# Kernel tuning notes

Measured on AMD Instinct MI355X. Metric: run time of the kernel, lower is better.

Reference implementation:

```python
import jax, jax.numpy as jnp
import numpy as np

BN_EPS = 1e-5


def conv1x1(x, W, b):
    # x: [B, Cin, N], W: [Cout, Cin], b: [Cout]
    return jnp.einsum('bcn,oc->bon', x, W) + b[None, :, None]


def batchnorm(x, gamma, beta):
    # training-mode BatchNorm1d over (batch, spatial) for x: [B, C, N]
    m = jnp.mean(x, axis=(0, 2), keepdims=True)
    v = jnp.var(x, axis=(0, 2), keepdims=True)
    return (x - m) * jax.lax.rsqrt(v + BN_EPS) * gamma[None, :, None] + beta[None, :, None]


def square_distance(a, b):
    # a: [B, N, 3], b: [B, S, 3] -> [B, N, S]
    aa = jnp.sum(a * a, axis=-1, keepdims=True)        # [B,N,1]
    bb = jnp.sum(b * b, axis=-1)[:, None, :]           # [B,1,S]
    return aa + bb - 2.0 * jnp.einsum('bnc,bsc->bns', a, b)


def setup_inputs() -> dict:
    key = jax.random.key(0)
    ks = jax.random.split(key, 16)
    B, N, S = 4, 8192, 2048
    D1, D2 = 128, 256
    Cin, Cout = D1 + D2, 256
    hid = Cout  # res_expansion = 1.0
    inp = {
        'xyz1': jax.random.normal(ks[0], (B, N, 3), jnp.float32),
        'xyz2': jax.random.normal(ks[1], (B, S, 3), jnp.float32),
        'points1': jax.random.normal(ks[2], (B, D1, N), jnp.float32),
        'points2': jax.random.normal(ks[3], (B, D2, S), jnp.float32),
        # fuse: Conv1d(Cin->Cout,k=1) + BN + ReLU
        'W_fuse': jax.random.normal(ks[4], (Cout, Cin), jnp.float32) * (1.0 / np.sqrt(Cin)),
        'b_fuse': jnp.zeros((Cout,), jnp.float32),
        'g_fuse': jnp.ones((Cout,), jnp.float32),
        'be_fuse': jnp.zeros((Cout,), jnp.float32),
        # extraction residual block: conv1 -> bn -> relu -> conv2 -> bn, +res, relu
        'W1': jax.random.normal(ks[5], (hid, Cout), jnp.float32) * (1.0 / np.sqrt(Cout)),
        'b1': jnp.zeros((hid,), jnp.float32),
        'g1': jnp.ones((hid,), jnp.float32),
        'be1': jnp.zeros((hid,), jnp.float32),
        'W2': jax.random.normal(ks[6], (Cout, hid), jnp.float32) * (1.0 / np.sqrt(hid)),
        'b2': jnp.zeros((Cout,), jnp.float32),
        'g2': jnp.ones((Cout,), jnp.float32),
        'be2': jnp.zeros((Cout,), jnp.float32),
    }
    return inp


def reference(xyz1, xyz2, points1, points2,
              W_fuse, b_fuse, g_fuse, be_fuse,
              W1, b1, g1, be1, W2, b2, g2, be2):
    B, N, _ = xyz1.shape
    p2 = jnp.transpose(points2, (0, 2, 1))  # [B, S, D2]
    # 3-NN inverse-distance interpolation
    dists = square_distance(xyz1, xyz2)                 # [B, N, S]
    neg_d3, idx = jax.lax.top_k(-dists, 3)              # 3 smallest distances
    d3 = -neg_d3                                        # [B, N, 3]
    recip = 1.0 / (d3 + 1e-8)
    weight = recip / jnp.sum(recip, axis=2, keepdims=True)  # [B, N, 3]
    gathered = jax.vmap(lambda pts, i: pts[i])(p2, idx)     # [B, N, 3, D2]
    interp = jnp.sum(gathered * weight[..., None], axis=2)  # [B, N, D2]
    # concat skip features
    p1 = jnp.transpose(points1, (0, 2, 1))              # [B, N, D1]
    new_points = jnp.concatenate([p1, interp], axis=-1) # [B, N, D1+D2]
    x = jnp.transpose(new_points, (0, 2, 1))            # [B, Cin, N]
    # fuse: ConvBNReLU1D
    x = jax.nn.relu(batchnorm(conv1x1(x, W_fuse, b_fuse), g_fuse, be_fuse))
    # extraction: residual ConvBNReLURes1D block
    y = jax.nn.relu(batchnorm(conv1x1(x, W1, b1), g1, be1))
    y = batchnorm(conv1x1(y, W2, b2), g2, be2)
    return jax.nn.relu(x + y)
```

## Files before the change

kernel.cpp:

```cpp
#include <hip/hip_runtime.h>
#include <cstdint>
#include <cstddef>

#define B_ 4
#define N_ 8192
#define S_ 2048
#define M_ 32768

typedef short bf16x8 __attribute__((ext_vector_type(8)));
typedef float f32x4 __attribute__((ext_vector_type(4)));

__device__ __forceinline__ float bf2f(unsigned short u) {
  union { unsigned int i; float f; } v; v.i = ((unsigned int)u) << 16; return v.f;
}
__device__ __forceinline__ unsigned short f2bf(float f) {
  union { float f; unsigned int i; } v; v.f = f;
  return (unsigned short)((v.i + 0x7FFFu + ((v.i >> 16) & 1u)) >> 16);
}

__global__ void pack_weights(const float* __restrict__ Wf, const float* __restrict__ W1,
                             const float* __restrict__ W2, unsigned short* __restrict__ out) {
  int i = blockIdx.x * 256 + threadIdx.x;
  float v;
  if (i < 98304)       v = Wf[i];
  else if (i < 163840) v = W1[i - 98304];
  else                 v = W2[i - 163840];
  out[i] = f2bf(v);
}

__global__ void transpose_to_bf16(const float* __restrict__ src, unsigned short* __restrict__ dst,
                                  int C, int Nsp, int ldo, int coff) {
  __shared__ float t[32][33];
  int b = blockIdx.z;
  int n0 = blockIdx.x * 32, c0 = blockIdx.y * 32;
  int x = threadIdx.x, y = threadIdx.y;
  const float* s = src + ((size_t)b * C + c0) * Nsp + n0;
#pragma unroll
  for (int k = 0; k < 4; ++k)
    t[y + k * 8][x] = s[(size_t)(y + k * 8) * Nsp + x];
  __syncthreads();
#pragma unroll
  for (int k = 0; k < 4; ++k) {
    int n = n0 + y + k * 8;
    dst[((size_t)b * Nsp + n) * ldo + coff + c0 + x] = f2bf(t[x][y + k * 8]);
  }
}

__device__ __forceinline__ bool lexlt(float da, int ia, float db, int ib) {
  return (da < db) || (da == db && ia < ib);
}

__global__ __launch_bounds__(256, 8) void knn_interp_kernel(
    const float* __restrict__ xyz1, const float* __restrict__ xyz2,
    const unsigned short* __restrict__ p2t, unsigned short* __restrict__ np) {
  __shared__ float4 sp[1024];
  __shared__ float sw[16][3];
  __shared__ int   sidx[16][3];
  int t = threadIdx.x;
  int b = blockIdx.y;
  const float* xb = xyz2 + (size_t)b * S_ * 3;

  int lane = t & 63, wave = t >> 6;
  int sub = lane & 15;
  int pib = wave * 4 + (lane >> 4);
  int n = blockIdx.x * 16 + pib;
  const float* q = xyz1 + ((size_t)b * N_ + n) * 3;
  float px = q[0], py = q[1], pz = q[2];
  float nx = -2.f * px, ny = -2.f * py, nz = -2.f * pz;
  float aa = fmaf(px, px, fmaf(py, py, pz * pz));

  float d0 = 1e30f, d1 = 1e30f, d2 = 1e30f;
  int i0 = S_, i1 = S_, i2 = S_;

  for (int chunk = 0; chunk < 2; ++chunk) {
    __syncthreads();
    for (int i = t; i < 1024; i += 256) {
      int c = chunk * 1024 + i;
      float cx = xb[3 * c], cy = xb[3 * c + 1], cz = xb[3 * c + 2];
      sp[i] = make_float4(cx, cy, cz, fmaf(cx, cx, fmaf(cy, cy, cz * cz)));
    }
    __syncthreads();
    int sbase = chunk * 1024;
#pragma unroll 4
    for (int i = 0; i < 64; ++i) {
      int sl = i * 16 + sub;
      float4 c = sp[sl];
      float d = fmaf(nx, c.x, fmaf(ny, c.y, fmaf(nz, c.z, c.w)));
      int s = sbase + sl;
      bool b0 = d < d0, b1 = d < d1, b2 = d < d2;
      d2 = b1 ? d1 : (b2 ? d : d2);
      i2 = b1 ? i1 : (b2 ? s : i2);
      d1 = b0 ? d0 : (b1 ? d : d1);
      i1 = b0 ? i0 : (b1 ? s : i1);
      d0 = b0 ? d : d0;
      i0 = b0 ? s : i0;
    }
  }

#pragma unroll
  for (int m = 1; m <= 8; m <<= 1) {
    float e0 = __shfl_xor(d0, m, 64), e1 = __shfl_xor(d1, m, 64), e2 = __shfl_xor(d2, m, 64);
    int   j0 = __shfl_xor(i0, m, 64), j1 = __shfl_xor(i1, m, 64), j2 = __shfl_xor(i2, m, 64);
    bool l0 = lexlt(d0, i0, e0, j0);
    float m0d = l0 ? d0 : e0;  int m0i = l0 ? i0 : j0;
    float x0d = l0 ? e0 : d0;  int x0i = l0 ? j0 : i0;
    bool l11 = lexlt(d1, i1, e1, j1);
    float n1d = l11 ? d1 : e1; int n1i = l11 ? i1 : j1;
    bool l1 = lexlt(n1d, n1i, x0d, x0i);
    float m1d = l1 ? n1d : x0d; int m1i = l1 ? n1i : x0i;
    bool l01 = lexlt(d0, i0, e1, j1);
    float p1d = l01 ? e1 : d0; int p1i = l01 ? j1 : i0;
    bool l10 = lexlt(d1, i1, e0, j0);
    float p2d = l10 ? e0 : d1; int p2i = l10 ? j0 : i1;
    bool lp = lexlt(p1d, p1i, p2d, p2i);
    float p3d = lp ? p1d : p2d; int p3i = lp ? p1i : p2i;
    bool l22 = lexlt(d2, i2, e2, j2);
    float p4d = l22 ? d2 : e2; int p4i = l22 ? i2 : j2;
    bool l2 = lexlt(p3d, p3i, p4d, p4i);
    float m2d = l2 ? p3d : p4d; int m2i = l2 ? p3i : p4i;
    d0 = m0d; i0 = m0i; d1 = m1d; i1 = m1i; d2 = m2d; i2 = m2i;
  }

  if (sub == 0) {
    float t0 = aa + d0, t1 = aa + d1, t2 = aa + d2;
    float r0 = 1.f / (t0 + 1e-8f), r1 = 1.f / (t1 + 1e-8f), r2 = 1.f / (t2 + 1e-8f);
    float rs = 1.f / (r0 + r1 + r2);
    sw[pib][0] = r0 * rs; sw[pib][1] = r1 * rs; sw[pib][2] = r2 * rs;
    sidx[pib][0] = i0; sidx[pib][1] = i1; sidx[pib][2] = i2;
  }
  __syncthreads();

  for (int p = wave; p < 16; p += 4) {
    float w0 = sw[p][0], w1 = sw[p][1], w2 = sw[p][2];
    const ushort4* g0 = (const ushort4*)(p2t + ((size_t)b * S_ + sidx[p][0]) * 256) + lane;
    const ushort4* g1 = (const ushort4*)(p2t + ((size_t)b * S_ + sidx[p][1]) * 256) + lane;
    const ushort4* g2 = (const ushort4*)(p2t + ((size_t)b * S_ + sidx[p][2]) * 256) + lane;
    ushort4 a = *g0, c = *g1, e = *g2;
    ushort4 o;
    o.x = f2bf(w0 * bf2f(a.x) + w1 * bf2f(c.x) + w2 * bf2f(e.x));
    o.y = f2bf(w0 * bf2f(a.y) + w1 * bf2f(c.y) + w2 * bf2f(e.y));
    o.z = f2bf(w0 * bf2f(a.z) + w1 * bf2f(c.z) + w2 * bf2f(e.z));
    o.w = f2bf(w0 * bf2f(a.w) + w1 * bf2f(c.w) + w2 * bf2f(e.w));
    int nn = blockIdx.x * 16 + p;
    *((ushort4*)(np + ((size_t)b * N_ + nn) * 384 + 128) + lane) = o;
  }
}

__global__ __launch_bounds__(256) void gemm_bt(const unsigned short* __restrict__ A,
                                               const unsigned short* __restrict__ Bw,
                                               float* __restrict__ C, int K) {
  __shared__ unsigned short As[128 * 64];
  __shared__ unsigned short Bs[128 * 64];
  int tid = threadIdx.x;
  int lane = tid & 63, wave = tid >> 6;
  int wr = wave >> 1, wc = wave & 1;
  size_t m0 = (size_t)blockIdx.x * 128;
  int n0 = blockIdx.y * 128;
  int lr = lane & 15, lk = lane >> 4;
  f32x4 acc[4][4] = {};

  for (int kt = 0; kt < K; kt += 64) {
#pragma unroll
    for (int i = 0; i < 4; ++i) {
      int ch = i * 256 + tid;
      int row = ch >> 3;
      int col = (ch & 7) * 8;
      __builtin_amdgcn_global_load_lds(
          (const __attribute__((address_space(1))) void*)(A + (m0 + row) * K + kt + col),
          (__attribute__((address_space(3))) void*)(As + ch * 8), 16, 0, 0);
    }
#pragma unroll
    for (int i = 0; i < 4; ++i) {
      int ch = i * 256 + tid;
      int row = ch >> 3;
      int col = (ch & 7) * 8;
      __builtin_amdgcn_global_load_lds(
          (const __attribute__((address_space(1))) void*)(Bw + (size_t)(n0 + row) * K + kt + col),
          (__attribute__((address_space(3))) void*)(Bs + ch * 8), 16, 0, 0);
    }
    __syncthreads();

    bf16x8 af[4][2], bf[4][2];
#pragma unroll
    for (int m = 0; m < 4; ++m)
#pragma unroll
      for (int kk = 0; kk < 2; ++kk)
        af[m][kk] = *(const bf16x8*)(As + (wr * 64 + m * 16 + lr) * 64 + kk * 32 + lk * 8);
#pragma unroll
    for (int nn = 0; nn < 4; ++nn)
#pragma unroll
      for (int kk = 0; kk < 2; ++kk)
        bf[nn][kk] = *(const bf16x8*)(Bs + (wc * 64 + nn * 16 + lr) * 64 + kk * 32 + lk * 8);

#pragma unroll
    for (int m = 0; m < 4; ++m)
#pragma unroll
      for (int nn = 0; nn < 4; ++nn)
#pragma unroll
        for (int kk = 0; kk < 2; ++kk)
          acc[m][nn] = __builtin_amdgcn_mfma_f32_16x16x32_bf16(af[m][kk], bf[nn][kk], acc[m][nn], 0, 0, 0);
    __syncthreads();
  }

#pragma unroll
  for (int m = 0; m < 4; ++m) {
    size_t row = m0 + wr * 64 + m * 16 + lk * 4;
#pragma unroll
    for (int j = 0; j < 4; ++j) {
      float* cr = C + (row + j) * 256 + n0 + wc * 64 + lr;
#pragma unroll
      for (int nn = 0; nn < 4; ++nn)
        cr[nn * 16] = acc[m][nn][j];
    }
  }
}

__global__ void col_stats(const float* __restrict__ X, float* __restrict__ sums) {
  int c = threadIdx.x;
  size_t r0 = (size_t)blockIdx.x * 256;
  float s0 = 0, s1 = 0, s2 = 0, s3 = 0, q0 = 0, q1 = 0, q2 = 0, q3 = 0;
  for (int r = 0; r < 256; r += 4) {
    float v0 = X[(r0 + r + 0) * 256 + c];
    float v1 = X[(r0 + r + 1) * 256 + c];
    float v2 = X[(r0 + r + 2) * 256 + c];
    float v3 = X[(r0 + r + 3) * 256 + c];
    s0 += v0; q0 += v0 * v0;
    s1 += v1; q1 += v1 * v1;
    s2 += v2; q2 += v2 * v2;
    s3 += v3; q3 += v3 * v3;
  }
  atomicAdd(&sums[c], s0 + s1 + s2 + s3);
  atomicAdd(&sums[256 + c], q0 + q1 + q2 + q3);
}

__global__ void bn_relu_kernel(const float* __restrict__ X, const float* __restrict__ sums,
                               const float* __restrict__ g, const float* __restrict__ be,
                               unsigned short* __restrict__ Y) {
  __shared__ float sc[256], sh[256];
  int t = threadIdx.x;
  {
    float s = sums[t], q = sums[256 + t];
    float m = s * (1.0f / 32768.0f);
    float v = q * (1.0f / 32768.0f) - m * m;
    float scale = g[t] * rsqrtf(v + 1e-5f);
    sc[t] = scale; sh[t] = be[t] - m * scale;
  }
  __syncthreads();
  const float4* X4 = (const float4*)X;
  ushort4* Y4 = (ushort4*)Y;
  for (size_t i = (size_t)blockIdx.x * 256 + t; i < (size_t)M_ * 64; i += 2048 * 256) {
    float4 x = X4[i];
    int c0 = (int)((i * 4) & 255);
    ushort4 o;
    o.x = f2bf(fmaxf(x.x * sc[c0 + 0] + sh[c0 + 0], 0.f));
    o.y = f2bf(fmaxf(x.y * sc[c0 + 1] + sh[c0 + 1], 0.f));
    o.z = f2bf(fmaxf(x.z * sc[c0 + 2] + sh[c0 + 2], 0.f));
    o.w = f2bf(fmaxf(x.w * sc[c0 + 3] + sh[c0 + 3], 0.f));
    Y4[i] = o;
  }
}

__global__ void final_kernel(const float* __restrict__ Z, const unsigned short* __restrict__ Xb,
                             const float* __restrict__ sums2, const float* __restrict__ g2,
                             const float* __restrict__ be2, float* __restrict__ out) {
  __shared__ float sc[64], sh[64];
  __shared__ float tile[64 * 65];
  int t = threadIdx.x;
  int o0 = blockIdx.y * 64;
  if (t < 64) {
    int c = o0 + t;
    float s = sums2[c], q = sums2[256 + c];
    float m = s * (1.0f / 32768.0f);
    float v = q * (1.0f / 32768.0f) - m * m;
    float scale = g2[c] * rsqrtf(v + 1e-5f);
    sc[t] = scale; sh[t] = be2[c] - m * scale;
  }
  __syncthreads();
  size_t m0 = (size_t)blockIdx.x * 64;
  int rl = t >> 4, cq = t & 15;
#pragma unroll
  for (int rr = 0; rr < 4; ++rr) {
    int row = rr * 16 + rl;
    size_t base = (m0 + row) * 256 + o0 + cq * 4;
    float4 z = *(const float4*)(Z + base);
    ushort4 x = *(const ushort4*)(Xb + base);
    int c = cq * 4;
    tile[row * 65 + c + 0] = fmaxf(z.x * sc[c + 0] + sh[c + 0] + bf2f(x.x), 0.f);
    tile[row * 65 + c + 1] = fmaxf(z.y * sc[c + 1] + sh[c + 1] + bf2f(x.y), 0.f);
    tile[row * 65 + c + 2] = fmaxf(z.z * sc[c + 2] + sh[c + 2] + bf2f(x.z), 0.f);
    tile[row * 65 + c + 3] = fmaxf(z.w * sc[c + 3] + sh[c + 3] + bf2f(x.w), 0.f);
  }
  __syncthreads();
  int b = (int)(m0 >> 13);
  int nbase = (int)(m0 & 8191);
  int orow = t >> 4, nq = t & 15;
#pragma unroll
  for (int ov = 0; ov < 4; ++ov) {
    int o = ov * 16 + orow;
    float4 v;
    v.x = tile[(nq * 4 + 0) * 65 + o];
    v.y = tile[(nq * 4 + 1) * 65 + o];
    v.z = tile[(nq * 4 + 2) * 65 + o];
    v.w = tile[(nq * 4 + 3) * 65 + o];
    *(float4*)(out + ((size_t)(b * 256 + o0 + o)) * 8192 + nbase + nq * 4) = v;
  }
}

extern "C" void kernel_launch(void* const* d_in, const int* in_sizes, int n_in,
                              void* d_out, int out_size, void* d_ws, size_t ws_size,
                              hipStream_t stream) {
  const float* xyz1    = (const float*)d_in[0];
  const float* xyz2    = (const float*)d_in[1];
  const float* points1 = (const float*)d_in[2];
  const float* points2 = (const float*)d_in[3];
  const float* W_fuse  = (const float*)d_in[4];
  const float* g_fuse  = (const float*)d_in[6];
  const float* be_fuse = (const float*)d_in[7];
  const float* W1      = (const float*)d_in[8];
  const float* g1      = (const float*)d_in[10];
  const float* be1     = (const float*)d_in[11];
  const float* W2      = (const float*)d_in[12];
  const float* g2      = (const float*)d_in[14];
  const float* be2     = (const float*)d_in[15];
  float* out = (float*)d_out;

  char* ws = (char*)d_ws;
  float* lin = (float*)ws;                   ws += (size_t)M_ * 256 * 4;
  unsigned short* xb = (unsigned short*)ws;  ws += (size_t)M_ * 256 * 2;
  unsigned short* np = (unsigned short*)ws;  ws += (size_t)M_ * 384 * 2;
  unsigned short* yb = np;
  unsigned short* p2t = (unsigned short*)ws; ws += (size_t)B_ * S_ * 256 * 2;
  unsigned short* wb = (unsigned short*)ws;  ws += 229376 * 2;
  float* stats = (float*)ws;

  hipMemsetAsync(stats, 0, 6 * 256 * sizeof(float), stream);
  pack_weights<<<896, 256, 0, stream>>>(W_fuse, W1, W2, wb);
  transpose_to_bf16<<<dim3(256, 4, 4), dim3(32, 8), 0, stream>>>(points1, np, 128, N_, 384, 0);
  transpose_to_bf16<<<dim3(64, 8, 4), dim3(32, 8), 0, stream>>>(points2, p2t, 256, S_, 256, 0);
  knn_interp_kernel<<<dim3(N_ / 16, B_), 256, 0, stream>>>(xyz1, xyz2, p2t, np);
  gemm_bt<<<dim3(M_ / 128, 2), 256, 0, stream>>>(np, wb, lin, 384);
  col_stats<<<128, 256, 0, stream>>>(lin, stats);
  bn_relu_kernel<<<2048, 256, 0, stream>>>(lin, stats, g_fuse, be_fuse, xb);
  gemm_bt<<<dim3(M_ / 128, 2), 256, 0, stream>>>(xb, wb + 98304, lin, 256);
  col_stats<<<128, 256, 0, stream>>>(lin, stats + 512);
  bn_relu_kernel<<<2048, 256, 0, stream>>>(lin, stats + 512, g1, be1, yb);
  gemm_bt<<<dim3(M_ / 128, 2), 256, 0, stream>>>(yb, wb + 163840, lin, 256);
  col_stats<<<128, 256, 0, stream>>>(lin, stats + 1024);
  final_kernel<<<dim3(M_ / 64, 4), 256, 0, stream>>>(lin, xb, stats + 1024, g2, be2, out);
}
```

Before: 161.8 us.

## Process four query points per thread in KNN kernel, use fmed3 top-3 insert

```diff
diff --git a/kernel.cpp b/kernel.cpp
--- a/kernel.cpp
+++ b/kernel.cpp
@@ -50,27 +50,39 @@
   return (da < db) || (da == db && ia < ib);
 }
 
-__global__ __launch_bounds__(256, 8) void knn_interp_kernel(
+__global__ __launch_bounds__(256) void knn_interp_kernel(
     const float* __restrict__ xyz1, const float* __restrict__ xyz2,
     const unsigned short* __restrict__ p2t, unsigned short* __restrict__ np) {
   __shared__ float4 sp[1024];
-  __shared__ float sw[16][3];
-  __shared__ int   sidx[16][3];
+  __shared__ float sw[64][3];
+  __shared__ int   sidx[64][3];
   int t = threadIdx.x;
-  int b = blockIdx.y;
+  int bx = blockIdx.x;
+  int b = bx >> 7;
   const float* xb = xyz2 + (size_t)b * S_ * 3;
 
   int lane = t & 63, wave = t >> 6;
   int sub = lane & 15;
-  int pib = wave * 4 + (lane >> 4);
-  int n = blockIdx.x * 16 + pib;
-  const float* q = xyz1 + ((size_t)b * N_ + n) * 3;
-  float px = q[0], py = q[1], pz = q[2];
-  float nx = -2.f * px, ny = -2.f * py, nz = -2.f * pz;
-  float aa = fmaf(px, px, fmaf(py, py, pz * pz));
-
-  float d0 = 1e30f, d1 = 1e30f, d2 = 1e30f;
-  int i0 = S_, i1 = S_, i2 = S_;
+  int qquad = lane >> 4;
+  int qloc = wave * 16 + qquad * 4;
+  size_t gq0 = (size_t)b * N_ + (size_t)(bx & 127) * 64 + qloc;
+
+  float px[4], py[4], pz[4], nx[4], ny[4], nz[4], aa[4];
+#pragma unroll
+  for (int k = 0; k < 4; ++k) {
+    const float* q = xyz1 + (gq0 + k) * 3;
+    px[k] = q[0]; py[k] = q[1]; pz[k] = q[2];
+    nx[k] = -2.f * px[k]; ny[k] = -2.f * py[k]; nz[k] = -2.f * pz[k];
+    aa[k] = fmaf(px[k], px[k], fmaf(py[k], py[k], pz[k] * pz[k]));
+  }
+
+  float d0[4], d1[4], d2[4];
+  int i0[4], i1[4], i2[4];
+#pragma unroll
+  for (int k = 0; k < 4; ++k) {
+    d0[k] = 1e30f; d1[k] = 1e30f; d2[k] = 1e30f;
+    i0[k] = S_; i1[k] = S_; i2[k] = S_;
+  }
 
   for (int chunk = 0; chunk < 2; ++chunk) {
     __syncthreads();
@@ -81,56 +93,67 @@
     }
     __syncthreads();
     int sbase = chunk * 1024;
-#pragma unroll 4
+#pragma unroll 2
     for (int i = 0; i < 64; ++i) {
       int sl = i * 16 + sub;
       float4 c = sp[sl];
-      float d = fmaf(nx, c.x, fmaf(ny, c.y, fmaf(nz, c.z, c.w)));
       int s = sbase + sl;
-      bool b0 = d < d0, b1 = d < d1, b2 = d < d2;
-      d2 = b1 ? d1 : (b2 ? d : d2);
-      i2 = b1 ? i1 : (b2 ? s : i2);
-      d1 = b0 ? d0 : (b1 ? d : d1);
-      i1 = b0 ? i0 : (b1 ? s : i1);
-      d0 = b0 ? d : d0;
-      i0 = b0 ? s : i0;
-    }
-  }
-
-#pragma unroll
-  for (int m = 1; m <= 8; m <<= 1) {
-    float e0 = __shfl_xor(d0, m, 64), e1 = __shfl_xor(d1, m, 64), e2 = __shfl_xor(d2, m, 64);
-    int   j0 = __shfl_xor(i0, m, 64), j1 = __shfl_xor(i1, m, 64), j2 = __shfl_xor(i2, m, 64);
-    bool l0 = lexlt(d0, i0, e0, j0);
-    float m0d = l0 ? d0 : e0;  int m0i = l0 ? i0 : j0;
-    float x0d = l0 ? e0 : d0;  int x0i = l0 ? j0 : i0;
-    bool l11 = lexlt(d1, i1, e1, j1);
-    float n1d = l11 ? d1 : e1; int n1i = l11 ? i1 : j1;
-    bool l1 = lexlt(n1d, n1i, x0d, x0i);
-    float m1d = l1 ? n1d : x0d; int m1i = l1 ? n1i : x0i;
-    bool l01 = lexlt(d0, i0, e1, j1);
-    float p1d = l01 ? e1 : d0; int p1i = l01 ? j1 : i0;
-    bool l10 = lexlt(d1, i1, e0, j0);
-    float p2d = l10 ? e0 : d1; int p2i = l10 ? j0 : i1;
-    bool lp = lexlt(p1d, p1i, p2d, p2i);
-    float p3d = lp ? p1d : p2d; int p3i = lp ? p1i : p2i;
-    bool l22 = lexlt(d2, i2, e2, j2);
-    float p4d = l22 ? d2 : e2; int p4i = l22 ? i2 : j2;
-    bool l2 = lexlt(p3d, p3i, p4d, p4i);
-    float m2d = l2 ? p3d : p4d; int m2i = l2 ? p3i : p4i;
-    d0 = m0d; i0 = m0i; d1 = m1d; i1 = m1i; d2 = m2d; i2 = m2i;
+#pragma unroll
+      for (int k = 0; k < 4; ++k) {
+        float d = fmaf(nx[k], c.x, fmaf(ny[k], c.y, fmaf(nz[k], c.z, c.w)));
+        bool b0 = d < d0[k], b1 = d < d1[k], b2 = d < d2[k];
+        i2[k] = b1 ? i1[k] : (b2 ? s : i2[k]);
+        i1[k] = b0 ? i0[k] : (b1 ? s : i1[k]);
+        i0[k] = b0 ? s : i0[k];
+        float nd1 = __builtin_amdgcn_fmed3f(d, d0[k], d1[k]);
+        float nd2 = __builtin_amdgcn_fmed3f(d, d1[k], d2[k]);
+        d0[k] = fminf(d0[k], d);
+        d1[k] = nd1; d2[k] = nd2;
+      }
+    }
+  }
+
+#pragma unroll
+  for (int k = 0; k < 4; ++k) {
+#pragma unroll
+    for (int m = 1; m <= 8; m <<= 1) {
+      float e0 = __shfl_xor(d0[k], m, 64), e1 = __shfl_xor(d1[k], m, 64), e2 = __shfl_xor(d2[k], m, 64);
+      int   j0 = __shfl_xor(i0[k], m, 64), j1 = __shfl_xor(i1[k], m, 64), j2 = __shfl_xor(i2[k], m, 64);
+      bool l0 = lexlt(d0[k], i0[k], e0, j0);
+      float m0d = l0 ? d0[k] : e0;  int m0i = l0 ? i0[k] : j0;
+      float x0d = l0 ? e0 : d0[k];  int x0i = l0 ? j0 : i0[k];
+      bool l11 = lexlt(d1[k], i1[k], e1, j1);
+      float n1d = l11 ? d1[k] : e1; int n1i = l11 ? i1[k] : j1;
+      bool l1 = lexlt(n1d, n1i, x0d, x0i);
+      float m1d = l1 ? n1d : x0d; int m1i = l1 ? n1i : x0i;
+      bool l01 = lexlt(d0[k], i0[k], e1, j1);
+      float p1d = l01 ? e1 : d0[k]; int p1i = l01 ? j1 : i0[k];
+      bool l10 = lexlt(d1[k], i1[k], e0, j0);
+      float p2d = l10 ? e0 : d1[k]; int p2i = l10 ? j0 : i1[k];
+      bool lp = lexlt(p1d, p1i, p2d, p2i);
+      float p3d = lp ? p1d : p2d; int p3i = lp ? p1i : p2i;
+      bool l22 = lexlt(d2[k], i2[k], e2, j2);
+      float p4d = l22 ? d2[k] : e2; int p4i = l22 ? i2[k] : j2;
+      bool l2 = lexlt(p3d, p3i, p4d, p4i);
+      float m2d = l2 ? p3d : p4d; int m2i = l2 ? p3i : p4i;
+      d0[k] = m0d; i0[k] = m0i; d1[k] = m1d; i1[k] = m1i; d2[k] = m2d; i2[k] = m2i;
+    }
   }
 
   if (sub == 0) {
-    float t0 = aa + d0, t1 = aa + d1, t2 = aa + d2;
-    float r0 = 1.f / (t0 + 1e-8f), r1 = 1.f / (t1 + 1e-8f), r2 = 1.f / (t2 + 1e-8f);
-    float rs = 1.f / (r0 + r1 + r2);
-    sw[pib][0] = r0 * rs; sw[pib][1] = r1 * rs; sw[pib][2] = r2 * rs;
-    sidx[pib][0] = i0; sidx[pib][1] = i1; sidx[pib][2] = i2;
-  }
-  __syncthreads();
-
-  for (int p = wave; p < 16; p += 4) {
+#pragma unroll
+    for (int k = 0; k < 4; ++k) {
+      float t0 = aa[k] + d0[k], t1 = aa[k] + d1[k], t2 = aa[k] + d2[k];
+      float r0 = 1.f / (t0 + 1e-8f), r1 = 1.f / (t1 + 1e-8f), r2 = 1.f / (t2 + 1e-8f);
+      float rs = 1.f / (r0 + r1 + r2);
+      sw[qloc + k][0] = r0 * rs; sw[qloc + k][1] = r1 * rs; sw[qloc + k][2] = r2 * rs;
+      sidx[qloc + k][0] = i0[k]; sidx[qloc + k][1] = i1[k]; sidx[qloc + k][2] = i2[k];
+    }
+  }
+  __syncthreads();
+
+  size_t grow0 = (size_t)b * N_ + (size_t)(bx & 127) * 64;
+  for (int p = wave; p < 64; p += 4) {
     float w0 = sw[p][0], w1 = sw[p][1], w2 = sw[p][2];
     const ushort4* g0 = (const ushort4*)(p2t + ((size_t)b * S_ + sidx[p][0]) * 256) + lane;
     const ushort4* g1 = (const ushort4*)(p2t + ((size_t)b * S_ + sidx[p][1]) * 256) + lane;
@@ -141,8 +164,7 @@
     o.y = f2bf(w0 * bf2f(a.y) + w1 * bf2f(c.y) + w2 * bf2f(e.y));
     o.z = f2bf(w0 * bf2f(a.z) + w1 * bf2f(c.z) + w2 * bf2f(e.z));
     o.w = f2bf(w0 * bf2f(a.w) + w1 * bf2f(c.w) + w2 * bf2f(e.w));
-    int nn = blockIdx.x * 16 + p;
-    *((ushort4*)(np + ((size_t)b * N_ + nn) * 384 + 128) + lane) = o;
+    *((ushort4*)(np + (grow0 + p) * 384 + 128) + lane) = o;
   }
 }
 
@@ -337,7 +359,7 @@
   pack_weights<<<896, 256, 0, stream>>>(W_fuse, W1, W2, wb);
   transpose_to_bf16<<<dim3(256, 4, 4), dim3(32, 8), 0, stream>>>(points1, np, 128, N_, 384, 0);
   transpose_to_bf16<<<dim3(64, 8, 4), dim3(32, 8), 0, stream>>>(points2, p2t, 256, S_, 256, 0);
-  knn_interp_kernel<<<dim3(N_ / 16, B_), 256, 0, stream>>>(xyz1, xyz2, p2t, np);
+  knn_interp_kernel<<<512, 256, 0, stream>>>(xyz1, xyz2, p2t, np);
   gemm_bt<<<dim3(M_ / 128, 2), 256, 0, stream>>>(np, wb, lin, 384);
   col_stats<<<128, 256, 0, stream>>>(lin, stats);
   bn_relu_kernel<<<2048, 256, 0, stream>>>(lin, stats, g_fuse, be_fuse, xb);
```

Result: slower. 187.2 us (+15.7%).
